# Optimization experiments

Measured on AMD Instinct MI355X. Metric: run time of the kernel, lower is better.

## Reference

```python
import jax, jax.numpy as jnp
import numpy as np

BS, N, XC, K, YS = 64, 1024, 1024, 256, 768

def setup_inputs() -> dict:
    key = jax.random.key(0)
    ks = jax.random.split(key, 5)
    return {
        "x": jax.random.normal(ks[0], (BS, N, XC), dtype=jnp.float32),
        "y": jax.random.normal(ks[1], (BS, YS), dtype=jnp.float32),
        "W_ch": jax.random.normal(ks[2], (K, XC), dtype=jnp.float32) * 0.02,
        "b_ch": jax.random.normal(ks[3], (K,), dtype=jnp.float32) * 0.02,
        "W_y": jax.random.normal(ks[4], (K, YS), dtype=jnp.float32) * 0.02,
    }

def reference(x, y, W_ch, b_ch, W_y):
    # y_k: [bs, k] (no bias)
    y_k = jnp.einsum('bs,ks->bk', y, W_y)
    # channel affine on every spatial position, batched: [bs, n, k]
    x_k = jnp.einsum('bnc,kc->bnk', x, W_ch) + b_ch
    # add per-sample y_k (broadcast over spatial dim), tanh, softmax over k
    z = jnp.tanh(x_k + y_k[:, None, :])
    attn = jax.nn.softmax(z, axis=-1)
    # torch.cat over dim=0 of per-sample [n, k] blocks -> [bs*n, k]
    return attn.reshape(-1, attn.shape[-1])
```

## Files before the change

kernel.cpp:

```cpp
#include <hip/hip_runtime.h>


#define XC    1024
#define KOUT  256
#define NT    16
#define LDSZ  16384

typedef float        f32x4_t  __attribute__((ext_vector_type(4)));
typedef unsigned int u32x4_t  __attribute__((ext_vector_type(4)));
typedef unsigned int u32x2_t  __attribute__((ext_vector_type(2)));
typedef __bf16       bf16x8_t __attribute__((ext_vector_type(8)));

__device__ __forceinline__ unsigned short f2bf(float f) {
  unsigned int u = __float_as_uint(f);
  u += 0x7fffu + ((u >> 16) & 1u);
  return (unsigned short)(u >> 16);
}

__device__ __forceinline__ float fast_tanh(float v) {
  float e = __expf(2.0f * v);
  return 1.0f - 2.0f / (e + 1.0f);
}

#define LGKM_BARRIER() do {                                  \
    asm volatile("s_waitcnt lgkmcnt(0)" ::: "memory");       \
    __builtin_amdgcn_s_barrier();                            \
    __builtin_amdgcn_sched_barrier(0);                       \
  } while (0)

__global__ void prep_kernel(const float* __restrict__ Wch,
                            const float* __restrict__ y,
                            const float* __restrict__ Wy,
                            const float* __restrict__ bch,
                            unsigned short* __restrict__ wbf,
                            float* __restrict__ biasws) {
  if (blockIdx.x < 256) {
    const int k = blockIdx.x;
    const int u = threadIdx.x;
    f32x4_t v = ((const f32x4_t*)(Wch + k * XC))[u];
    const int c0   = u << 2;
    const int t    = c0 >> 6;
    const int ch   = (c0 & 63) >> 3;
    const int kk   = ch >> 2;
    const int lg   = ch & 3;
    const int half = (c0 >> 2) & 1;
    const int wv   = k >> 6;
    const int ni   = (k >> 4) & 3;
    const int lr   = k & 15;
    const int lane = (lg << 4) | lr;
    unsigned int lo = (unsigned int)f2bf(v.x) | ((unsigned int)f2bf(v.y) << 16);
    unsigned int hi = (unsigned int)f2bf(v.z) | ((unsigned int)f2bf(v.w) << 16);
    char* p = (char*)wbf +
              ((size_t)((((t << 2) + wv) * 2 + kk) * 4 + ni) << 10) +
              (lane << 4) + (half << 3);
    *(u32x2_t*)p = (u32x2_t){lo, hi};
  } else {
    __shared__ __align__(16) float ys[768];
    const int b = blockIdx.x - 256;
    const int k = threadIdx.x;
    for (int i = k; i < 768; i += 256) ys[i] = y[b * 768 + i];
    __syncthreads();
    const f32x4_t* w4 = (const f32x4_t*)(Wy + k * 768);
    const f32x4_t* y4 = (const f32x4_t*)ys;
    float s = 0.f;
#pragma unroll 8
    for (int i = 0; i < 192; ++i) {
      f32x4_t w = w4[i], a = y4[i];
      s = fmaf(w.x, a.x, s); s = fmaf(w.y, a.y, s);
      s = fmaf(w.z, a.z, s); s = fmaf(w.w, a.w, s);
    }
    biasws[b * 256 + k] = s + bch[k];
  }
}

__global__ __launch_bounds__(256, 2) void fused_kernel(
    const float* __restrict__ x, const unsigned short* __restrict__ wbf,
    const float* __restrict__ bias, float* __restrict__ out) {
  __shared__ __align__(16) unsigned char smem[LDSZ];
  const int tid = threadIdx.x;
  const int l   = tid & 63;
  const int wv  = tid >> 6;
  const int lr  = l & 15;
  const int lg  = l >> 4;
  const int m0  = blockIdx.x << 6;
  const int bidx = m0 >> 10;
  const int rr  = tid >> 4;
  const int c4  = tid & 15;

  f32x4_t acc[4][4];
#pragma unroll
  for (int i = 0; i < 4; ++i)
#pragma unroll
    for (int j = 0; j < 4; ++j) acc[i][j] = (f32x4_t){0.f, 0.f, 0.f, 0.f};

  const float* xb = x + (size_t)m0 * XC + (size_t)rr * XC + (c4 << 2);
  const char* wsrc = (const char*)wbf;
  f32x4_t avA[4], avB[4];
  bf16x8_t bfr[8];

#define LOADA(dst, tt) do {                                                  \
    _Pragma("unroll")                                                        \
    for (int j = 0; j < 4; ++j)                                              \
      dst[j] = *(const f32x4_t*)(xb + (size_t)(j << 4) * XC + ((tt) << 6));  \
  } while (0)

#define LOADB(tt) do {                                                       \
    const char* g = wsrc + (size_t)(tt) * 32768 + (wv << 13) + (l << 4);     \
    _Pragma("unroll")                                                        \
    for (int f = 0; f < 8; ++f)                                              \
      bfr[f] = __builtin_bit_cast(bf16x8_t, *(const u32x4_t*)(g + (f << 10)));\
  } while (0)

#define WRITEA(src, buf) do {                                                \
    _Pragma("unroll")                                                        \
    for (int j = 0; j < 4; ++j) {                                            \
      const int row = (j << 4) + rr;                                         \
      unsigned int lo = (unsigned int)f2bf(src[j].x) |                       \
                        ((unsigned int)f2bf(src[j].y) << 16);                \
      unsigned int hi = (unsigned int)f2bf(src[j].z) |                       \
                        ((unsigned int)f2bf(src[j].w) << 16);                \
      char* p = (char*)smem + ((buf) << 13) + row * 128 +                    \
                (((c4 >> 1) ^ (row & 7)) << 4) + ((c4 & 1) << 3);            \
      *(u32x2_t*)p = (u32x2_t){lo, hi};                                      \
    }                                                                        \
  } while (0)

#define COMPUTE(buf) do {                                                    \
    const u32x4_t* aB = (const u32x4_t*)(smem + ((buf) << 13));              \
    _Pragma("unroll")                                                        \
    for (int kk = 0; kk < 2; ++kk) {                                         \
      const int cs = ((kk << 2) | lg) ^ (lr & 7);                            \
      bf16x8_t afr[4];                                                       \
      _Pragma("unroll")                                                      \
      for (int mi = 0; mi < 4; ++mi)                                         \
        afr[mi] = __builtin_bit_cast(bf16x8_t, aB[(((mi << 4) + lr) << 3) + cs]);\
      _Pragma("unroll")                                                      \
      for (int mi = 0; mi < 4; ++mi)                                         \
        _Pragma("unroll")                                                    \
        for (int nj = 0; nj < 4; ++nj)                                       \
          acc[mi][nj] = __builtin_amdgcn_mfma_f32_16x16x32_bf16(             \
              afr[mi], bfr[(kk << 2) | nj], acc[mi][nj], 0, 0, 0);           \
    }                                                                        \
  } while (0)

  LOADA(avA, 0);
  LOADA(avB, 1);
  LOADB(0);
  WRITEA(avA, 0);
  LGKM_BARRIER();

  for (int t = 0; t < NT; t += 2) {
    if (t + 2 < NT) LOADA(avA, t + 2);
    COMPUTE(0);
    if (t + 1 < NT) LOADB(t + 1);
    if (t + 1 < NT) WRITEA(avB, 1);
    LGKM_BARRIER();
    if (t + 3 < NT) LOADA(avB, t + 3);
    COMPUTE(1);
    if (t + 2 < NT) LOADB(t + 2);
    if (t + 2 < NT) WRITEA(avA, 0);
    if (t + 2 < NT) LGKM_BARRIER();
  }
  __syncthreads();

#undef LOADA
#undef LOADB
#undef WRITEA
#undef COMPUTE

  float* wred    = (float*)smem;
  float* rowstat = (float*)(smem + 1024);

  float brow[4];
#pragma unroll
  for (int ni = 0; ni < 4; ++ni)
    brow[ni] = bias[(bidx << 8) + (wv << 6) + (ni << 4) + lr];

#pragma unroll
  for (int mi = 0; mi < 4; ++mi)
#pragma unroll
    for (int ni = 0; ni < 4; ++ni)
#pragma unroll
      for (int r = 0; r < 4; ++r)
        acc[mi][ni][r] = fast_tanh(acc[mi][ni][r] + brow[ni]);

#pragma unroll
  for (int mi = 0; mi < 4; ++mi)
#pragma unroll
    for (int r = 0; r < 4; ++r) {
      float m = fmaxf(fmaxf(acc[mi][0][r], acc[mi][1][r]),
                      fmaxf(acc[mi][2][r], acc[mi][3][r]));
      m = fmaxf(m, __shfl_xor(m, 1));
      m = fmaxf(m, __shfl_xor(m, 2));
      m = fmaxf(m, __shfl_xor(m, 4));
      m = fmaxf(m, __shfl_xor(m, 8));
      if (lr == 0) wred[(wv << 6) + (mi << 4) + (lg << 2) + r] = m;
    }
  __syncthreads();
  if (tid < 64)
    rowstat[tid] = fmaxf(fmaxf(wred[tid], wred[64 + tid]),
                         fmaxf(wred[128 + tid], wred[192 + tid]));
  __syncthreads();

#pragma unroll
  for (int mi = 0; mi < 4; ++mi)
#pragma unroll
    for (int r = 0; r < 4; ++r) {
      const int row = (mi << 4) + (lg << 2) + r;
      const float m = rowstat[row];
      float s = 0.f;
#pragma unroll
      for (int ni = 0; ni < 4; ++ni) {
        float e = __expf(acc[mi][ni][r] - m);
        acc[mi][ni][r] = e;
        s += e;
      }
      s += __shfl_xor(s, 1);
      s += __shfl_xor(s, 2);
      s += __shfl_xor(s, 4);
      s += __shfl_xor(s, 8);
      if (lr == 0) wred[(wv << 6) + row] = s;
    }
  __syncthreads();
  if (tid < 64)
    rowstat[tid] = 1.0f / (wred[tid] + wred[64 + tid] +
                           wred[128 + tid] + wred[192 + tid]);
  __syncthreads();

#pragma unroll
  for (int mi = 0; mi < 4; ++mi)
#pragma unroll
    for (int r = 0; r < 4; ++r) {
      const int row = (mi << 4) + (lg << 2) + r;
      const float rinv = rowstat[row];
      float* orow = out + (size_t)(m0 + row) * KOUT + (wv << 6) + lr;
#pragma unroll
      for (int ni = 0; ni < 4; ++ni)
        orow[ni << 4] = acc[mi][ni][r] * rinv;
    }
}

extern "C" void kernel_launch(void* const* d_in, const int* in_sizes, int n_in,
                              void* d_out, int out_size, void* d_ws, size_t ws_size,
                              hipStream_t stream) {
  (void)in_sizes; (void)n_in; (void)out_size; (void)ws_size;
  const float* x   = (const float*)d_in[0];
  const float* y   = (const float*)d_in[1];
  const float* Wch = (const float*)d_in[2];
  const float* bch = (const float*)d_in[3];
  const float* Wy  = (const float*)d_in[4];
  float* out = (float*)d_out;
  unsigned short* wbf = (unsigned short*)d_ws;
  float* biasws = (float*)((char*)d_ws + 512 * 1024);

  hipLaunchKernelGGL(prep_kernel, dim3(320), dim3(256), 0, stream,
                     Wch, y, Wy, bch, wbf, biasws);
  hipLaunchKernelGGL(fused_kernel, dim3(1024), dim3(256), 0, stream,
                     x, wbf, biasws, out);
}
```

Baseline: 117.5 us.

## Split N dimension across 8 waves per block and double-buffer B fragments

The fused GEMM+softmax block grows from 4 to 8 waves (512 threads), each wave computing a 64x32 output slice instead of 64x64. This halves per-thread accumulators and staging registers, which should allow higher occupancy and more latency hiding. B fragments are now double-buffered in registers (bfrA/bfrB) and issued earlier so global loads overlap with MFMA work. The cost is that the cross-wave softmax reductions now combine 8 partials, and each block issues more synchronisation traffic.

Result: slower. 123.5 us (+5.1%).

```diff
diff --git a/kernel.cpp b/kernel.cpp
--- a/kernel.cpp
+++ b/kernel.cpp
@@ -73,13 +73,15 @@
   }
 }
 
-__global__ __launch_bounds__(256, 2) void fused_kernel(
+__global__ __launch_bounds__(512, 4) void fused_kernel(
     const float* __restrict__ x, const unsigned short* __restrict__ wbf,
     const float* __restrict__ bias, float* __restrict__ out) {
   __shared__ __align__(16) unsigned char smem[LDSZ];
   const int tid = threadIdx.x;
   const int l   = tid & 63;
-  const int wv  = tid >> 6;
+  const int w   = tid >> 6;
+  const int wv2 = w >> 1;
+  const int nh  = w & 1;
   const int lr  = l & 15;
   const int lg  = l >> 4;
   const int m0  = blockIdx.x << 6;
@@ -87,34 +89,37 @@
   const int rr  = tid >> 4;
   const int c4  = tid & 15;
 
-  f32x4_t acc[4][4];
+  f32x4_t acc[4][2];
 #pragma unroll
   for (int i = 0; i < 4; ++i)
 #pragma unroll
-    for (int j = 0; j < 4; ++j) acc[i][j] = (f32x4_t){0.f, 0.f, 0.f, 0.f};
+    for (int j = 0; j < 2; ++j) acc[i][j] = (f32x4_t){0.f, 0.f, 0.f, 0.f};
 
   const float* xb = x + (size_t)m0 * XC + (size_t)rr * XC + (c4 << 2);
-  const char* wsrc = (const char*)wbf;
-  f32x4_t avA[4], avB[4];
-  bf16x8_t bfr[8];
+  const char* wsrc = (const char*)wbf + (wv2 << 13) + (nh << 11) + (l << 4);
+  f32x4_t avA[2], avB[2];
+  bf16x8_t bfrA[4], bfrB[4];
 
 #define LOADA(dst, tt) do {                                                  \
     _Pragma("unroll")                                                        \
-    for (int j = 0; j < 4; ++j)                                              \
-      dst[j] = *(const f32x4_t*)(xb + (size_t)(j << 4) * XC + ((tt) << 6));  \
-  } while (0)
-
-#define LOADB(tt) do {                                                       \
-    const char* g = wsrc + (size_t)(tt) * 32768 + (wv << 13) + (l << 4);     \
-    _Pragma("unroll")                                                        \
-    for (int f = 0; f < 8; ++f)                                              \
-      bfr[f] = __builtin_bit_cast(bf16x8_t, *(const u32x4_t*)(g + (f << 10)));\
+    for (int j = 0; j < 2; ++j)                                              \
+      dst[j] = *(const f32x4_t*)(xb + (size_t)(j << 5) * XC + ((tt) << 6));  \
+  } while (0)
+
+#define LOADB(dst, tt) do {                                                  \
+    const char* g = wsrc + (size_t)(tt) * 32768;                             \
+    _Pragma("unroll")                                                        \
+    for (int kk = 0; kk < 2; ++kk)                                           \
+      _Pragma("unroll")                                                      \
+      for (int nj = 0; nj < 2; ++nj)                                         \
+        dst[(kk << 1) | nj] = __builtin_bit_cast(bf16x8_t,                   \
+            *(const u32x4_t*)(g + (((kk << 2) | nj) << 10)));                \
   } while (0)
 
 #define WRITEA(src, buf) do {                                                \
     _Pragma("unroll")                                                        \
-    for (int j = 0; j < 4; ++j) {                                            \
-      const int row = (j << 4) + rr;                                         \
+    for (int j = 0; j < 2; ++j) {                                            \
+      const int row = (j << 5) + rr;                                         \
       unsigned int lo = (unsigned int)f2bf(src[j].x) |                       \
                         ((unsigned int)f2bf(src[j].y) << 16);                \
       unsigned int hi = (unsigned int)f2bf(src[j].z) |                       \
@@ -125,7 +130,7 @@
     }                                                                        \
   } while (0)
 
-#define COMPUTE(buf) do {                                                    \
+#define COMPUTE(buf, bsrc) do {                                              \
     const u32x4_t* aB = (const u32x4_t*)(smem + ((buf) << 13));              \
     _Pragma("unroll")                                                        \
     for (int kk = 0; kk < 2; ++kk) {                                         \
@@ -137,27 +142,27 @@
       _Pragma("unroll")                                                      \
       for (int mi = 0; mi < 4; ++mi)                                         \
         _Pragma("unroll")                                                    \
-        for (int nj = 0; nj < 4; ++nj)                                       \
+        for (int nj = 0; nj < 2; ++nj)                                       \
           acc[mi][nj] = __builtin_amdgcn_mfma_f32_16x16x32_bf16(             \
-              afr[mi], bfr[(kk << 2) | nj], acc[mi][nj], 0, 0, 0);           \
+              afr[mi], bsrc[(kk << 1) | nj], acc[mi][nj], 0, 0, 0);          \
     }                                                                        \
   } while (0)
 
+  LOADB(bfrA, 0);
   LOADA(avA, 0);
   LOADA(avB, 1);
-  LOADB(0);
   WRITEA(avA, 0);
   LGKM_BARRIER();
 
   for (int t = 0; t < NT; t += 2) {
+    if (t + 1 < NT) LOADB(bfrB, t + 1);
     if (t + 2 < NT) LOADA(avA, t + 2);
-    COMPUTE(0);
-    if (t + 1 < NT) LOADB(t + 1);
+    COMPUTE(0, bfrA);
     if (t + 1 < NT) WRITEA(avB, 1);
     LGKM_BARRIER();
+    if (t + 2 < NT) LOADB(bfrA, t + 2);
     if (t + 3 < NT) LOADA(avB, t + 3);
-    COMPUTE(1);
-    if (t + 2 < NT) LOADB(t + 2);
+    COMPUTE(1, bfrB);
     if (t + 2 < NT) WRITEA(avA, 0);
     if (t + 2 < NT) LGKM_BARRIER();
   }
@@ -169,37 +174,39 @@
 #undef COMPUTE
 
   float* wred    = (float*)smem;
-  float* rowstat = (float*)(smem + 1024);
-
-  float brow[4];
-#pragma unroll
-  for (int ni = 0; ni < 4; ++ni)
-    brow[ni] = bias[(bidx << 8) + (wv << 6) + (ni << 4) + lr];
-
-#pragma unroll
-  for (int mi = 0; mi < 4; ++mi)
-#pragma unroll
-    for (int ni = 0; ni < 4; ++ni)
+  float* rowstat = (float*)(smem + 2048);
+
+  float brow[2];
+#pragma unroll
+  for (int nj = 0; nj < 2; ++nj)
+    brow[nj] = bias[(bidx << 8) + (w << 5) + (nj << 4) + lr];
+
+#pragma unroll
+  for (int mi = 0; mi < 4; ++mi)
+#pragma unroll
+    for (int nj = 0; nj < 2; ++nj)
 #pragma unroll
       for (int r = 0; r < 4; ++r)
-        acc[mi][ni][r] = fast_tanh(acc[mi][ni][r] + brow[ni]);
+        acc[mi][nj][r] = fast_tanh(acc[mi][nj][r] + brow[nj]);
 
 #pragma unroll
   for (int mi = 0; mi < 4; ++mi)
 #pragma unroll
     for (int r = 0; r < 4; ++r) {
-      float m = fmaxf(fmaxf(acc[mi][0][r], acc[mi][1][r]),
-                      fmaxf(acc[mi][2][r], acc[mi][3][r]));
+      float m = fmaxf(acc[mi][0][r], acc[mi][1][r]);
       m = fmaxf(m, __shfl_xor(m, 1));
       m = fmaxf(m, __shfl_xor(m, 2));
       m = fmaxf(m, __shfl_xor(m, 4));
       m = fmaxf(m, __shfl_xor(m, 8));
-      if (lr == 0) wred[(wv << 6) + (mi << 4) + (lg << 2) + r] = m;
-    }
-  __syncthreads();
-  if (tid < 64)
-    rowstat[tid] = fmaxf(fmaxf(wred[tid], wred[64 + tid]),
-                         fmaxf(wred[128 + tid], wred[192 + tid]));
+      if (lr == 0) wred[(w << 6) + (mi << 4) + (lg << 2) + r] = m;
+    }
+  __syncthreads();
+  if (tid < 64) {
+    float m = wred[tid];
+#pragma unroll
+    for (int ww = 1; ww < 8; ++ww) m = fmaxf(m, wred[(ww << 6) + tid]);
+    rowstat[tid] = m;
+  }
   __syncthreads();
 
 #pragma unroll
@@ -210,21 +217,24 @@
       const float m = rowstat[row];
       float s = 0.f;
 #pragma unroll
-      for (int ni = 0; ni < 4; ++ni) {
-        float e = __expf(acc[mi][ni][r] - m);
-        acc[mi][ni][r] = e;
+      for (int nj = 0; nj < 2; ++nj) {
+        float e = __expf(acc[mi][nj][r] - m);
+        acc[mi][nj][r] = e;
         s += e;
       }
       s += __shfl_xor(s, 1);
       s += __shfl_xor(s, 2);
       s += __shfl_xor(s, 4);
       s += __shfl_xor(s, 8);
-      if (lr == 0) wred[(wv << 6) + row] = s;
-    }
-  __syncthreads();
-  if (tid < 64)
-    rowstat[tid] = 1.0f / (wred[tid] + wred[64 + tid] +
-                           wred[128 + tid] + wred[192 + tid]);
+      if (lr == 0) wred[(w << 6) + row] = s;
+    }
+  __syncthreads();
+  if (tid < 64) {
+    float s = wred[tid];
+#pragma unroll
+    for (int ww = 1; ww < 8; ++ww) s += wred[(ww << 6) + tid];
+    rowstat[tid] = 1.0f / s;
+  }
   __syncthreads();
 
 #pragma unroll
@@ -233,10 +243,10 @@
     for (int r = 0; r < 4; ++r) {
       const int row = (mi << 4) + (lg << 2) + r;
       const float rinv = rowstat[row];
-      float* orow = out + (size_t)(m0 + row) * KOUT + (wv << 6) + lr;
-#pragma unroll
-      for (int ni = 0; ni < 4; ++ni)
-        orow[ni << 4] = acc[mi][ni][r] * rinv;
+      float* orow = out + (size_t)(m0 + row) * KOUT + (w << 5) + lr;
+#pragma unroll
+      for (int nj = 0; nj < 2; ++nj)
+        orow[nj << 4] = acc[mi][nj][r] * rinv;
     }
 }
 
@@ -255,6 +265,6 @@
 
   hipLaunchKernelGGL(prep_kernel, dim3(320), dim3(256), 0, stream,
                      Wch, y, Wy, bch, wbf, biasws);
-  hipLaunchKernelGGL(fused_kernel, dim3(1024), dim3(256), 0, stream,
+  hipLaunchKernelGGL(fused_kernel, dim3(1024), dim3(512), 0, stream,
                      x, wbf, biasws, out);
 }
```

## Stream x tiles into LDS via async global_load_lds with triple buffering

Applied to the files above, without the earlier changes.

Replaces the register-staged load, bf16 convert and LDS write of x with direct global-to-LDS async copies of raw fp32 into a three-stage ring buffer. The bf16 conversion moves to after the LDS read in the compute step, and B fragments are double-buffered in registers. The goal is to take the A staging through registers off the critical path and get deeper prefetch with vmcnt-based waits. In exchange it uses three times the LDS (48KB, fp32 tiles), adds conversion work per LDS read, and raises the occupancy target to 3 blocks per CU.

After: 130.8 us. +11.2%, slower.

```diff
diff --git a/kernel.cpp b/kernel.cpp
--- a/kernel.cpp
+++ b/kernel.cpp
@@ -4,7 +4,8 @@
 #define XC    1024
 #define KOUT  256
 #define NT    16
-#define LDSZ  16384
+#define ABSZ  16384
+#define LDSZ  49152
 
 typedef float        f32x4_t  __attribute__((ext_vector_type(4)));
 typedef unsigned int u32x4_t  __attribute__((ext_vector_type(4)));
@@ -22,11 +23,13 @@
   return 1.0f - 2.0f / (e + 1.0f);
 }
 
-#define LGKM_BARRIER() do {                                  \
-    asm volatile("s_waitcnt lgkmcnt(0)" ::: "memory");       \
-    __builtin_amdgcn_s_barrier();                            \
-    __builtin_amdgcn_sched_barrier(0);                       \
-  } while (0)
+__device__ __forceinline__ void async_copy16(const void* lds, const void* g) {
+  __builtin_amdgcn_global_load_lds(
+      (const __attribute__((address_space(1))) void*)g,
+      (__attribute__((address_space(3))) void*)lds, 16, 0, 0);
+}
+
+#define PIPE_WAIT(N) asm volatile("s_waitcnt vmcnt(" #N ")" ::: "memory")
 
 __global__ void prep_kernel(const float* __restrict__ Wch,
                             const float* __restrict__ y,
@@ -73,19 +76,17 @@
   }
 }
 
-__global__ __launch_bounds__(256, 2) void fused_kernel(
+__global__ __launch_bounds__(256, 3) void fused_kernel(
     const float* __restrict__ x, const unsigned short* __restrict__ wbf,
     const float* __restrict__ bias, float* __restrict__ out) {
   __shared__ __align__(16) unsigned char smem[LDSZ];
   const int tid = threadIdx.x;
   const int l   = tid & 63;
-  const int wv  = tid >> 6;
+  const int w   = tid >> 6;
   const int lr  = l & 15;
   const int lg  = l >> 4;
   const int m0  = blockIdx.x << 6;
   const int bidx = m0 >> 10;
-  const int rr  = tid >> 4;
-  const int c4  = tid & 15;
 
   f32x4_t acc[4][4];
 #pragma unroll
@@ -93,79 +94,75 @@
 #pragma unroll
     for (int j = 0; j < 4; ++j) acc[i][j] = (f32x4_t){0.f, 0.f, 0.f, 0.f};
 
-  const float* xb = x + (size_t)m0 * XC + (size_t)rr * XC + (c4 << 2);
-  const char* wsrc = (const char*)wbf;
-  f32x4_t avA[4], avB[4];
-  bf16x8_t bfr[8];
-
-#define LOADA(dst, tt) do {                                                  \
+  const char* xbase = (const char*)x + ((size_t)m0 << 12);
+  const char* wsrc  = (const char*)wbf + (w << 13) + (l << 4);
+  bf16x8_t bfrA[8], bfrB[8];
+
+#define DMA_A(tt, buf) do {                                                  \
     _Pragma("unroll")                                                        \
-    for (int j = 0; j < 4; ++j)                                              \
-      dst[j] = *(const f32x4_t*)(xb + (size_t)(j << 4) * XC + ((tt) << 6));  \
+    for (int i = 0; i < 4; ++i) {                                            \
+      const int row = (w << 4) + (i << 2) + (l >> 4);                        \
+      const int sw  = ((l >> 1) & 7) ^ (row & 7);                            \
+      const char* g = xbase + ((size_t)row << 12) + ((tt) << 8) +            \
+                      (sw << 5) + ((l & 1) << 4);                            \
+      async_copy16(smem + (buf) * ABSZ + (w << 12) + (i << 10), g);          \
+    }                                                                        \
   } while (0)
 
-#define LOADB(tt) do {                                                       \
-    const char* g = wsrc + (size_t)(tt) * 32768 + (wv << 13) + (l << 4);     \
+#define LOADB(dst, tt) do {                                                  \
+    const char* g = wsrc + (size_t)(tt) * 32768;                             \
     _Pragma("unroll")                                                        \
     for (int f = 0; f < 8; ++f)                                              \
-      bfr[f] = __builtin_bit_cast(bf16x8_t, *(const u32x4_t*)(g + (f << 10)));\
+      dst[f] = __builtin_bit_cast(bf16x8_t, *(const u32x4_t*)(g + (f << 10)));\
   } while (0)
 
-#define WRITEA(src, buf) do {                                                \
-    _Pragma("unroll")                                                        \
-    for (int j = 0; j < 4; ++j) {                                            \
-      const int row = (j << 4) + rr;                                         \
-      unsigned int lo = (unsigned int)f2bf(src[j].x) |                       \
-                        ((unsigned int)f2bf(src[j].y) << 16);                \
-      unsigned int hi = (unsigned int)f2bf(src[j].z) |                       \
-                        ((unsigned int)f2bf(src[j].w) << 16);                \
-      char* p = (char*)smem + ((buf) << 13) + row * 128 +                    \
-                (((c4 >> 1) ^ (row & 7)) << 4) + ((c4 & 1) << 3);            \
-      *(u32x2_t*)p = (u32x2_t){lo, hi};                                      \
-    }                                                                        \
-  } while (0)
-
-#define COMPUTE(buf) do {                                                    \
-    const u32x4_t* aB = (const u32x4_t*)(smem + ((buf) << 13));              \
+#define COMPUTE(bufc, bsrc) do {                                             \
+    const f32x4_t* aB = (const f32x4_t*)(smem + (bufc) * ABSZ);              \
     _Pragma("unroll")                                                        \
     for (int kk = 0; kk < 2; ++kk) {                                         \
-      const int cs = ((kk << 2) | lg) ^ (lr & 7);                            \
       bf16x8_t afr[4];                                                       \
       _Pragma("unroll")                                                      \
-      for (int mi = 0; mi < 4; ++mi)                                         \
-        afr[mi] = __builtin_bit_cast(bf16x8_t, aB[(((mi << 4) + lr) << 3) + cs]);\
+      for (int mi = 0; mi < 4; ++mi) {                                       \
+        const int row = (mi << 4) + lr;                                      \
+        const int sw  = (((kk << 2) | lg) ^ (row & 7));                      \
+        f32x4_t lo = aB[(row << 4) + (sw << 1)];                             \
+        f32x4_t hi = aB[(row << 4) + (sw << 1) + 1];                         \
+        bf16x8_t t_;                                                         \
+        t_[0] = (__bf16)lo.x; t_[1] = (__bf16)lo.y;                          \
+        t_[2] = (__bf16)lo.z; t_[3] = (__bf16)lo.w;                          \
+        t_[4] = (__bf16)hi.x; t_[5] = (__bf16)hi.y;                          \
+        t_[6] = (__bf16)hi.z; t_[7] = (__bf16)hi.w;                          \
+        afr[mi] = t_;                                                        \
+      }                                                                      \
       _Pragma("unroll")                                                      \
       for (int mi = 0; mi < 4; ++mi)                                         \
         _Pragma("unroll")                                                    \
         for (int nj = 0; nj < 4; ++nj)                                       \
           acc[mi][nj] = __builtin_amdgcn_mfma_f32_16x16x32_bf16(             \
-              afr[mi], bfr[(kk << 2) | nj], acc[mi][nj], 0, 0, 0);           \
+              afr[mi], bsrc[(kk << 2) | nj], acc[mi][nj], 0, 0, 0);          \
     }                                                                        \
   } while (0)
 
-  LOADA(avA, 0);
-  LOADA(avB, 1);
-  LOADB(0);
-  WRITEA(avA, 0);
-  LGKM_BARRIER();
-
-  for (int t = 0; t < NT; t += 2) {
-    if (t + 2 < NT) LOADA(avA, t + 2);
-    COMPUTE(0);
-    if (t + 1 < NT) LOADB(t + 1);
-    if (t + 1 < NT) WRITEA(avB, 1);
-    LGKM_BARRIER();
-    if (t + 3 < NT) LOADA(avB, t + 3);
-    COMPUTE(1);
-    if (t + 2 < NT) LOADB(t + 2);
-    if (t + 2 < NT) WRITEA(avA, 0);
-    if (t + 2 < NT) LGKM_BARRIER();
+  DMA_A(0, 0);
+  LOADB(bfrA, 0);
+  DMA_A(1, 1);
+
+#pragma unroll
+  for (int s = 0; s < NT; ++s) {
+    if (s < NT - 1) { PIPE_WAIT(4); } else { PIPE_WAIT(0); }
+    __builtin_amdgcn_sched_barrier(0);
+    __builtin_amdgcn_s_barrier();
+    __builtin_amdgcn_sched_barrier(0);
+    if (s + 1 < NT) {
+      if (s & 1) LOADB(bfrA, s + 1); else LOADB(bfrB, s + 1);
+    }
+    if (s + 2 < NT) DMA_A(s + 2, (s + 2) % 3);
+    if (s & 1) COMPUTE(s % 3, bfrB); else COMPUTE(s % 3, bfrA);
   }
   __syncthreads();
 
-#undef LOADA
+#undef DMA_A
 #undef LOADB
-#undef WRITEA
 #undef COMPUTE
 
   float* wred    = (float*)smem;
@@ -174,7 +171,7 @@
   float brow[4];
 #pragma unroll
   for (int ni = 0; ni < 4; ++ni)
-    brow[ni] = bias[(bidx << 8) + (wv << 6) + (ni << 4) + lr];
+    brow[ni] = bias[(bidx << 8) + (w << 6) + (ni << 4) + lr];
 
 #pragma unroll
   for (int mi = 0; mi < 4; ++mi)
@@ -194,7 +191,7 @@
       m = fmaxf(m, __shfl_xor(m, 2));
       m = fmaxf(m, __shfl_xor(m, 4));
       m = fmaxf(m, __shfl_xor(m, 8));
-      if (lr == 0) wred[(wv << 6) + (mi << 4) + (lg << 2) + r] = m;
+      if (lr == 0) wred[(w << 6) + (mi << 4) + (lg << 2) + r] = m;
     }
   __syncthreads();
   if (tid < 64)
@@ -219,7 +216,7 @@
       s += __shfl_xor(s, 2);
       s += __shfl_xor(s, 4);
       s += __shfl_xor(s, 8);
-      if (lr == 0) wred[(wv << 6) + row] = s;
+      if (lr == 0) wred[(w << 6) + row] = s;
     }
   __syncthreads();
   if (tid < 64)
@@ -233,7 +230,7 @@
     for (int r = 0; r < 4; ++r) {
       const int row = (mi << 4) + (lg << 2) + r;
       const float rinv = rowstat[row];
-      float* orow = out + (size_t)(m0 + row) * KOUT + (wv << 6) + lr;
+      float* orow = out + (size_t)(m0 + row) * KOUT + (w << 6) + lr;
 #pragma unroll
       for (int ni = 0; ni < 4; ++ni)
         orow[ni << 4] = acc[mi][ni][r] * rinv;
```

## Deepen software pipeline with triple-buffered A registers and double-buffered B fragments

Applied to the files above, without the earlier changes.

Restructures the main GEMM loop so global loads of x run three stages ahead in register slots, and weight fragments are double-buffered in registers and loaded one stage ahead, before the MFMA compute of the current stage. The loop is fully unrolled, and the launch bounds now request three blocks per CU instead of two. The aim is to hide global memory latency better and raise occupancy. The extra register buffers together with the tighter occupancy bound may force register spills or reduce scheduling freedom.

Result: slower. 204.1 us (+73.7%).

```diff
diff --git a/kernel.cpp b/kernel.cpp
--- a/kernel.cpp
+++ b/kernel.cpp
@@ -73,7 +73,7 @@
   }
 }
 
-__global__ __launch_bounds__(256, 2) void fused_kernel(
+__global__ __launch_bounds__(256, 3) void fused_kernel(
     const float* __restrict__ x, const unsigned short* __restrict__ wbf,
     const float* __restrict__ bias, float* __restrict__ out) {
   __shared__ __align__(16) unsigned char smem[LDSZ];
@@ -94,38 +94,38 @@
     for (int j = 0; j < 4; ++j) acc[i][j] = (f32x4_t){0.f, 0.f, 0.f, 0.f};
 
   const float* xb = x + (size_t)m0 * XC + (size_t)rr * XC + (c4 << 2);
-  const char* wsrc = (const char*)wbf;
-  f32x4_t avA[4], avB[4];
-  bf16x8_t bfr[8];
-
-#define LOADA(dst, tt) do {                                                  \
+  const char* wsrc = (const char*)wbf + (wv << 13) + (l << 4);
+  f32x4_t av[3][4];
+  bf16x8_t bfrA[8], bfrB[8];
+
+#define LOADA(slot, tt) do {                                                 \
     _Pragma("unroll")                                                        \
     for (int j = 0; j < 4; ++j)                                              \
-      dst[j] = *(const f32x4_t*)(xb + (size_t)(j << 4) * XC + ((tt) << 6));  \
-  } while (0)
-
-#define LOADB(tt) do {                                                       \
-    const char* g = wsrc + (size_t)(tt) * 32768 + (wv << 13) + (l << 4);     \
+      av[slot][j] = *(const f32x4_t*)(xb + (size_t)(j << 4) * XC + ((tt) << 6));\
+  } while (0)
+
+#define LOADB(dst, tt) do {                                                  \
+    const char* g = wsrc + (size_t)(tt) * 32768;                             \
     _Pragma("unroll")                                                        \
     for (int f = 0; f < 8; ++f)                                              \
-      bfr[f] = __builtin_bit_cast(bf16x8_t, *(const u32x4_t*)(g + (f << 10)));\
-  } while (0)
-
-#define WRITEA(src, buf) do {                                                \
+      dst[f] = __builtin_bit_cast(bf16x8_t, *(const u32x4_t*)(g + (f << 10)));\
+  } while (0)
+
+#define WRITEA(slot, buf) do {                                               \
     _Pragma("unroll")                                                        \
     for (int j = 0; j < 4; ++j) {                                            \
       const int row = (j << 4) + rr;                                         \
-      unsigned int lo = (unsigned int)f2bf(src[j].x) |                       \
-                        ((unsigned int)f2bf(src[j].y) << 16);                \
-      unsigned int hi = (unsigned int)f2bf(src[j].z) |                       \
-                        ((unsigned int)f2bf(src[j].w) << 16);                \
+      unsigned int lo = (unsigned int)f2bf(av[slot][j].x) |                  \
+                        ((unsigned int)f2bf(av[slot][j].y) << 16);           \
+      unsigned int hi = (unsigned int)f2bf(av[slot][j].z) |                  \
+                        ((unsigned int)f2bf(av[slot][j].w) << 16);           \
       char* p = (char*)smem + ((buf) << 13) + row * 128 +                    \
                 (((c4 >> 1) ^ (row & 7)) << 4) + ((c4 & 1) << 3);            \
       *(u32x2_t*)p = (u32x2_t){lo, hi};                                      \
     }                                                                        \
   } while (0)
 
-#define COMPUTE(buf) do {                                                    \
+#define COMPUTE(buf, bsrc) do {                                              \
     const u32x4_t* aB = (const u32x4_t*)(smem + ((buf) << 13));              \
     _Pragma("unroll")                                                        \
     for (int kk = 0; kk < 2; ++kk) {                                         \
@@ -139,27 +139,26 @@
         _Pragma("unroll")                                                    \
         for (int nj = 0; nj < 4; ++nj)                                       \
           acc[mi][nj] = __builtin_amdgcn_mfma_f32_16x16x32_bf16(             \
-              afr[mi], bfr[(kk << 2) | nj], acc[mi][nj], 0, 0, 0);           \
+              afr[mi], bsrc[(kk << 2) | nj], acc[mi][nj], 0, 0, 0);          \
     }                                                                        \
   } while (0)
 
-  LOADA(avA, 0);
-  LOADA(avB, 1);
-  LOADB(0);
-  WRITEA(avA, 0);
+  LOADB(bfrA, 0);
+  LOADA(0, 0);
+  LOADA(1, 1);
+  LOADA(2, 2);
+  WRITEA(0, 0);
   LGKM_BARRIER();
 
-  for (int t = 0; t < NT; t += 2) {
-    if (t + 2 < NT) LOADA(avA, t + 2);
-    COMPUTE(0);
-    if (t + 1 < NT) LOADB(t + 1);
-    if (t + 1 < NT) WRITEA(avB, 1);
-    LGKM_BARRIER();
-    if (t + 3 < NT) LOADA(avB, t + 3);
-    COMPUTE(1);
-    if (t + 2 < NT) LOADB(t + 2);
-    if (t + 2 < NT) WRITEA(avA, 0);
-    if (t + 2 < NT) LGKM_BARRIER();
+#pragma unroll
+  for (int s = 0; s < NT; ++s) {
+    if (s + 1 < NT) { if (s & 1) LOADB(bfrA, s + 1); else LOADB(bfrB, s + 1); }
+    if (s + 3 < NT) LOADA(s % 3, s + 3);
+    if (s & 1) COMPUTE(1, bfrB); else COMPUTE(0, bfrA);
+    if (s + 1 < NT) {
+      WRITEA((s + 1) % 3, (s + 1) & 1);
+      LGKM_BARRIER();
+    }
   }
   __syncthreads();
 
```
